# Kernel tuning notes

Hardware: AMD Instinct MI355X
Metric: run time of the kernel (lower is better)

## Reference

```python
import jax
jax.config.update("jax_enable_x64", True)
import jax.numpy as jnp
import numpy as np

N = 46337            # Paillier modulus n (chosen so n^2 fits in int32 range, products fit int64)
NSQ = N * N          # ciphertexts live in Z_{n^2}
POOL = (2, 2)        # pool_size == strides, padding='valid', channels_last


def setup_inputs() -> dict:
    key = jax.random.key(0)
    # Paillier ciphertexts: uniform big integers in [0, n^2)
    x = jax.random.randint(key, (32, 256, 256, 64), 0, NSQ, dtype=jnp.int64)
    return {"x": x}


def reference(x) -> jnp.ndarray:
    # Homomorphic sum-pooling over 2x2 windows:
    # Paillier: Enc(a) * Enc(b) mod n^2 == Enc(a + b), so windowed "sum" pooling
    # of encrypted values is a windowed modular PRODUCT of ciphertexts mod n^2.
    B, H, W, C = x.shape
    ph, pw = POOL
    Ho, Wo = H // ph, W // pw  # 'valid' padding, stride == pool_size
    # [B, Ho, ph, Wo, pw, C] non-overlapping windows via reshape
    xw = x[:, : Ho * ph, : Wo * pw, :].reshape(B, Ho, ph, Wo, pw, C)
    out = jnp.ones((B, Ho, Wo, C), dtype=x.dtype)
    for i in range(ph):          # fixed tiny window loop (4 iters), fully vectorized per iter
        for j in range(pw):
            out = (out * xw[:, :, i, :, j, :]) % NSQ  # modular product, stays < 2^63
    return out
```

## Files before the change

kernel.cpp:

```cpp
#include <hip/hip_runtime.h>


#define NSQ 2147117569ULL

typedef int int4v __attribute__((ext_vector_type(4)));

__global__ __launch_bounds__(256) void paillier_pool_kernel(
    const int* __restrict__ x, int* __restrict__ out, int nwork)
{
    const int stride = gridDim.x * blockDim.x;
    for (int wi = blockIdx.x * blockDim.x + threadIdx.x; wi < nwork; wi += stride) {
        int flat = wi << 2;
        int c  = flat & 63;
        int wo = (flat >> 6) & 127;
        int ho = (flat >> 13) & 127;
        int b  = flat >> 20;

        int base = (((b << 8) + (ho << 1) << 8) + (wo << 1)) * 64 + c;

        int4v v00 = __builtin_nontemporal_load((const int4v*)(x + base));
        int4v v01 = __builtin_nontemporal_load((const int4v*)(x + base + 64));
        int4v v10 = __builtin_nontemporal_load((const int4v*)(x + base + 16384));
        int4v v11 = __builtin_nontemporal_load((const int4v*)(x + base + 16384 + 64));

        int4v r;
#pragma unroll
        for (int k = 0; k < 4; ++k) {
            unsigned long long t0 = (unsigned long long)(unsigned)v00[k] * (unsigned)v01[k] % NSQ;
            unsigned long long t1 = (unsigned long long)(unsigned)v10[k] * (unsigned)v11[k] % NSQ;
            unsigned long long t  = (t0 * t1) % NSQ;
            r[k] = (int)(unsigned)t;
        }

        __builtin_nontemporal_store(r, (int4v*)(out + flat));
    }
}

extern "C" void kernel_launch(void* const* d_in, const int* in_sizes, int n_in,
                              void* d_out, int out_size, void* d_ws, size_t ws_size,
                              hipStream_t stream) {
    const int* x = (const int*)d_in[0];
    int* out = (int*)d_out;

    const int nwork = out_size / 4;
    const int block = 256;
    const int grid  = 2048;

    paillier_pool_kernel<<<grid, block, 0, stream>>>(x, out, nwork);
}
```

Measured before the change: 117.7 us.

## Replace 64-bit modulo with pseudo-Mersenne folding and process eight outputs per thread

Replaces the generic 64-bit unsigned modulo by NSQ, which is a slow software routine on GPU, with a reduction that uses 2^31 ≡ 366079 mod NSQ: three fold steps and one final conditional subtract. Each thread now handles eight channels instead of four, issuing eight 16-byte loads and two stores to raise memory-level parallelism. The intermediate values after folding may not be fully reduced before the next multiply, so correctness depends on the bounds holding within 32 bits.

```diff
diff --git a/kernel.cpp b/kernel.cpp
--- a/kernel.cpp
+++ b/kernel.cpp
@@ -1,38 +1,59 @@
 #include <hip/hip_runtime.h>
 
 
-#define NSQ 2147117569ULL
+#define M   2147117569u
+#define K31 366079ull
 
 typedef int int4v __attribute__((ext_vector_type(4)));
+
+__device__ __forceinline__ unsigned modmul31(unsigned a, unsigned b) {
+    unsigned long long p = (unsigned long long)a * b;
+    p = (unsigned long long)(unsigned)(p >> 31) * K31 + (unsigned)(p & 0x7FFFFFFF);
+    p = (unsigned long long)(unsigned)(p >> 31) * K31 + (unsigned)(p & 0x7FFFFFFF);
+    p = (unsigned long long)(unsigned)(p >> 31) * K31 + (unsigned)(p & 0x7FFFFFFF);
+    return (unsigned)p;
+}
 
 __global__ __launch_bounds__(256) void paillier_pool_kernel(
     const int* __restrict__ x, int* __restrict__ out, int nwork)
 {
     const int stride = gridDim.x * blockDim.x;
     for (int wi = blockIdx.x * blockDim.x + threadIdx.x; wi < nwork; wi += stride) {
-        int flat = wi << 2;
+        int flat = wi << 3;
         int c  = flat & 63;
         int wo = (flat >> 6) & 127;
         int ho = (flat >> 13) & 127;
         int b  = flat >> 20;
 
-        int base = (((b << 8) + (ho << 1) << 8) + (wo << 1)) * 64 + c;
+        int base = ((((b << 8) + (ho << 1)) << 8) + (wo << 1)) * 64 + c;
 
-        int4v v00 = __builtin_nontemporal_load((const int4v*)(x + base));
-        int4v v01 = __builtin_nontemporal_load((const int4v*)(x + base + 64));
-        int4v v10 = __builtin_nontemporal_load((const int4v*)(x + base + 16384));
-        int4v v11 = __builtin_nontemporal_load((const int4v*)(x + base + 16384 + 64));
+        int4v v00a = __builtin_nontemporal_load((const int4v*)(x + base));
+        int4v v00b = __builtin_nontemporal_load((const int4v*)(x + base + 4));
+        int4v v01a = __builtin_nontemporal_load((const int4v*)(x + base + 64));
+        int4v v01b = __builtin_nontemporal_load((const int4v*)(x + base + 68));
+        int4v v10a = __builtin_nontemporal_load((const int4v*)(x + base + 16384));
+        int4v v10b = __builtin_nontemporal_load((const int4v*)(x + base + 16388));
+        int4v v11a = __builtin_nontemporal_load((const int4v*)(x + base + 16448));
+        int4v v11b = __builtin_nontemporal_load((const int4v*)(x + base + 16452));
 
-        int4v r;
+        int4v ra, rb;
 #pragma unroll
         for (int k = 0; k < 4; ++k) {
-            unsigned long long t0 = (unsigned long long)(unsigned)v00[k] * (unsigned)v01[k] % NSQ;
-            unsigned long long t1 = (unsigned long long)(unsigned)v10[k] * (unsigned)v11[k] % NSQ;
-            unsigned long long t  = (t0 * t1) % NSQ;
-            r[k] = (int)(unsigned)t;
+            unsigned t0 = modmul31((unsigned)v00a[k], (unsigned)v01a[k]);
+            unsigned t1 = modmul31((unsigned)v10a[k], (unsigned)v11a[k]);
+            unsigned t  = modmul31(t0, t1);
+            if (t >= M) t -= M;
+            ra[k] = (int)t;
+
+            unsigned u0 = modmul31((unsigned)v00b[k], (unsigned)v01b[k]);
+            unsigned u1 = modmul31((unsigned)v10b[k], (unsigned)v11b[k]);
+            unsigned u  = modmul31(u0, u1);
+            if (u >= M) u -= M;
+            rb[k] = (int)u;
         }
 
-        __builtin_nontemporal_store(r, (int4v*)(out + flat));
+        __builtin_nontemporal_store(ra, (int4v*)(out + flat));
+        __builtin_nontemporal_store(rb, (int4v*)(out + flat + 4));
     }
 }
 
@@ -42,7 +63,7 @@
     const int* x = (const int*)d_in[0];
     int* out = (int*)d_out;
 
-    const int nwork = out_size / 4;
+    const int nwork = out_size / 8;
     const int block = 256;
     const int grid  = 2048;
 
```

New measurement: 148.7 us. 26.3% more time.
